# Optimization experiments

Hardware: AMD Instinct MI355X
Metric: run time of the kernel (lower is better)

The kernel has to match this reference:

```python
import jax, jax.numpy as jnp
import numpy as np

ACT_BIT = 3
W_BIT = 2


def fake_quant(x, bits):
    """Symmetric uniform fake-quantization to `bits` bits (dequantized values)."""
    qmax = float((1 << (bits - 1)) - 1)
    scale = jnp.max(jnp.abs(x)) / qmax
    scale = jnp.where(scale == 0, jnp.ones_like(scale), scale)
    return jnp.clip(jnp.round(x / scale), -qmax, qmax) * scale


def setup_inputs() -> dict:
    key = jax.random.key(0)
    kA, kX, kWi, kWo = jax.random.split(key, 4)
    N, D_IN, D_H, D_OUT = 8192, 128, 64, 16
    A = jax.random.normal(kA, (N, N), dtype=jnp.float32)       # dense subgraph adjacency (binarized inside)
    X = jax.random.normal(kX, (N, D_IN), dtype=jnp.float32)    # node features
    W_in = jax.random.normal(kWi, (D_IN, D_H), dtype=jnp.float32)
    W_out = jax.random.normal(kWo, (D_H, D_OUT), dtype=jnp.float32)
    return {"A": A, "X": X, "W_in": W_in, "W_out": W_out}


def reference(A, X, W_in, W_out):
    # QGTC GCNConv_Qnt: A quantized to 1 bit, activations to act_bit, weights to w_bit.
    Aq = (A > 0).astype(A.dtype)                 # 1-bit adjacency (bit_qnt(A, 1))
    Xq = fake_quant(X, ACT_BIT)                  # X_Qnt
    Wi = fake_quant(W_in, W_BIT)                 # weight_Qnt
    Wo = fake_quant(W_out, W_BIT)
    # Layer 1: mm_v1(X, W_in) then mm_v1(A, .) with output re-quantized to act_bit
    h = Aq @ (Xq @ Wi)                           # [N, D_H]
    hq = fake_quant(h, ACT_BIT)
    # Layer 2 (output layer)
    out = Aq @ (hq @ Wo)                         # [N, D_OUT]
    return out
```

## Files before the change

kernel.cpp:

```cpp
#include <hip/hip_runtime.h>

#define NN 8192
#define DIN 128
#define DH 64
#define DOUT 16
#define KS 8

typedef _Float16 half8 __attribute__((ext_vector_type(8)));
typedef float f32x4 __attribute__((ext_vector_type(4)));

#define OFF_SC    0u
#define OFF_PART  256u
#define OFF_YT    65536u
#define OFF_RT    1114112u
#define OFF_HF    1376256u
#define OFF_BITS  3473408u
#define OFF_P1    11862016u

__device__ __forceinline__ int permk(int k) {
  int e = k & 255;
  return (k & ~255) | (((e & 3) << 6) | (e >> 2));
}

__device__ __forceinline__ float getscale(const unsigned* sc, int idx, float qmax) {
  float s = __uint_as_float(sc[idx]) / qmax;
  return (s == 0.0f) ? 1.0f : s;
}

__device__ __forceinline__ half8 expand8(unsigned bb) {
  uint4 w;
  w.x = ((bb & 1u)  ? 0x3C00u : 0u) | ((bb & 2u)   ? 0x3C000000u : 0u);
  w.y = ((bb & 4u)  ? 0x3C00u : 0u) | ((bb & 8u)   ? 0x3C000000u : 0u);
  w.z = ((bb & 16u) ? 0x3C00u : 0u) | ((bb & 32u)  ? 0x3C000000u : 0u);
  w.w = ((bb & 64u) ? 0x3C00u : 0u) | ((bb & 128u) ? 0x3C000000u : 0u);
  return __builtin_bit_cast(half8, w);
}

__global__ __launch_bounds__(256) void k_scalesbits(const float* __restrict__ A,
                                                    const float* __restrict__ X,
                                                    const float* __restrict__ Wi,
                                                    const float* __restrict__ Wo,
                                                    unsigned char* __restrict__ bits,
                                                    unsigned* part, unsigned* sc) {
  const int t = threadIdx.x, bx = blockIdx.x;
  if (bx < 4096) {
    const int lane = t & 63, warp = t >> 6;
    const size_t wbase = ((size_t)bx * 4 + warp) * 4096;
    const float4* ap = (const float4*)(A + wbase) + lane;
    unsigned char* bp = bits + (wbase >> 3);
#pragma unroll
    for (int g = 0; g < 16; ++g) {
      float4 v = ap[g * 64];
      unsigned long long m0 = __ballot(v.x > 0.0f);
      unsigned long long m1 = __ballot(v.y > 0.0f);
      unsigned long long m2 = __ballot(v.z > 0.0f);
      unsigned long long m3 = __ballot(v.w > 0.0f);
      unsigned long long lo = (lane & 1) ? m1 : m0;
      unsigned long long hi = (lane & 1) ? m3 : m2;
      unsigned long long word = (lane & 2) ? hi : lo;
      if (lane < 4) *(unsigned long long*)(bp + g * 32 + lane * 8) = word;
    }
    return;
  }
  __shared__ float red[256];
  const int b = bx - 4096;
  float m = 0.0f;
  if (b < 240) {
    for (int i = b * 256 + t; i < NN * DIN; i += 240 * 256) m = fmaxf(m, fabsf(X[i]));
  } else if (b == 240) {
    for (int i = t; i < DIN * DH; i += 256) m = fmaxf(m, fabsf(Wi[i]));
    if (t == 0) sc[3] = 0u;
  } else {
    for (int i = t; i < DH * DOUT; i += 256) m = fmaxf(m, fabsf(Wo[i]));
  }
  red[t] = m; __syncthreads();
  for (int s = 128; s > 0; s >>= 1) {
    if (t < s) red[t] = fmaxf(red[t], red[t + s]);
    __syncthreads();
  }
  if (t == 0) part[b] = __float_as_uint(red[0]);
}

__global__ __launch_bounds__(256) void k_Y(const float* __restrict__ X,
                                           const float* __restrict__ Wi,
                                           const unsigned* __restrict__ part,
                                           unsigned* sc,
                                           _Float16* __restrict__ YT) {
  __shared__ float red[256];
  __shared__ float Xs[8][129];
  __shared__ float Ws[DIN][DH];
  const int t = threadIdx.x;
  red[t] = (t < 240) ? __uint_as_float(part[t]) : 0.0f;
  __syncthreads();
  for (int s = 128; s > 0; s >>= 1) {
    if (t < s) red[t] = fmaxf(red[t], red[t + s]);
    __syncthreads();
  }
  float sxraw = red[0];
  float sx = sxraw / 3.0f; sx = (sx == 0.0f) ? 1.0f : sx;
  float swi = __uint_as_float(part[240]); swi = (swi == 0.0f) ? 1.0f : swi;
  if (blockIdx.x == 0 && t == 0) sc[0] = __float_as_uint(sxraw);
  const int k0 = blockIdx.x * 8;
  __syncthreads();
  for (int i = t; i < 8 * DIN; i += 256) {
    int r = i >> 7, c = i & 127;
    float q = rintf(X[(size_t)(k0 + r) * DIN + c] / sx);
    Xs[r][c] = fminf(fmaxf(q, -3.0f), 3.0f);
  }
  for (int i = t; i < DIN * DH; i += 256) {
    float q = rintf(Wi[i] / swi);
    Ws[i >> 6][i & 63] = fminf(fmaxf(q, -1.0f), 1.0f);
  }
  __syncthreads();
  const int r = t & 7, jp = t >> 3, j = jp * 2;
  float a0 = 0.0f, a1 = 0.0f;
  for (int n = 0; n < DIN; ++n) {
    float xv = Xs[r][n];
    a0 = fmaf(xv, Ws[n][j], a0);
    a1 = fmaf(xv, Ws[n][j + 1], a1);
  }
  const int kp = permk(k0 + r);
  YT[(size_t)j * NN + kp]       = (_Float16)a0;
  YT[(size_t)(j + 1) * NN + kp] = (_Float16)a1;
}

__global__ __launch_bounds__(256) void k_gemm1(const unsigned char* __restrict__ bits,
                                               const _Float16* __restrict__ YT,
                                               float* __restrict__ P1) {
  __shared__ __align__(16) char Bs[64 * 128];
  const int t = threadIdx.x, lane = t & 63, warp = t >> 6;
  const int row0 = blockIdx.x * 128;
  const int split = blockIdx.y;
  const int l15 = lane & 15, lq = lane >> 4;
  const int sh8 = lq * 8;

  f32x4 acc[2][4] = {};

  const int bn = t >> 2, bp = t & 3;
  const _Float16* bsrc = YT + (size_t)bn * NN + split * 1024 + bp * 16;
  char* bdst0 = &Bs[bn * 128 + ((bp * 32) ^ ((bn & 7) << 4))];
  char* bdst1 = &Bs[bn * 128 + ((bp * 32 + 16) ^ ((bn & 7) << 4))];

  const unsigned char* brow0 = bits + (size_t)(row0 + warp * 32 + l15) * 1024 + split * 128;
  const unsigned char* brow1 = brow0 + 16 * 1024;

  uint4 breg0 = *(const uint4*)(bsrc);
  uint4 breg1 = *(const uint4*)(bsrc + 8);

  for (int it = 0; it < 16; ++it) {
    __syncthreads();
    *(uint4*)bdst0 = breg0;
    *(uint4*)bdst1 = breg1;
    if (it < 15) {
      breg0 = *(const uint4*)(bsrc + (it + 1) * 64);
      breg1 = *(const uint4*)(bsrc + (it + 1) * 64 + 8);
    }
    uint2 w0 = *(const uint2*)(brow0 + it * 8);
    uint2 w1 = *(const uint2*)(brow1 + it * 8);
    __syncthreads();
#pragma unroll
    for (int kk = 0; kk < 2; ++kk) {
      half8 af0 = expand8(((kk ? w0.y : w0.x) >> sh8) & 0xffu);
      half8 af1 = expand8(((kk ? w1.y : w1.x) >> sh8) & 0xffu);
#pragma unroll
      for (int n = 0; n < 4; ++n) {
        half8 bf = *(const half8*)(&Bs[(n * 16 + l15) * 128 +
                                       ((lq * 16 + kk * 64) ^ ((l15 & 7) << 4))]);
        acc[0][n] = __builtin_amdgcn_mfma_f32_16x16x32_f16(af0, bf, acc[0][n], 0, 0, 0);
        acc[1][n] = __builtin_amdgcn_mfma_f32_16x16x32_f16(af1, bf, acc[1][n], 0, 0, 0);
      }
    }
  }
  const int r4 = lq * 4;
#pragma unroll
  for (int mf = 0; mf < 2; ++mf) {
#pragma unroll
    for (int n = 0; n < 4; ++n) {
#pragma unroll
      for (int i = 0; i < 4; ++i) {
        int rr = row0 + warp * 32 + mf * 16 + r4 + i;
        int cc = n * 16 + l15;
        P1[((size_t)split * NN + rr) * DH + cc] = acc[mf][n][i];
      }
    }
  }
}

__global__ __launch_bounds__(256) void k_h2(const float* __restrict__ P1,
                                            const unsigned* __restrict__ part,
                                            unsigned* sc, float* __restrict__ hf) {
  float sx = getscale(sc, 0, 3.0f);
  float swi = __uint_as_float(part[240]); swi = (swi == 0.0f) ? 1.0f : swi;
  float sxw = sx * swi;
  int idx = blockIdx.x * 256 + threadIdx.x;
  const float4* p = (const float4*)P1;
  float4 s = {0, 0, 0, 0};
#pragma unroll
  for (int sp = 0; sp < KS; ++sp) {
    float4 v = p[(size_t)sp * (NN * DH / 4) + idx];
    s.x += v.x; s.y += v.y; s.z += v.z; s.w += v.w;
  }
  s.x *= sxw; s.y *= sxw; s.z *= sxw; s.w *= sxw;
  ((float4*)hf)[idx] = s;
  float m = fmaxf(fmaxf(fabsf(s.x), fabsf(s.y)), fmaxf(fabsf(s.z), fabsf(s.w)));
  __shared__ float red[256];
  red[threadIdx.x] = m; __syncthreads();
  for (int st = 128; st > 0; st >>= 1) {
    if (threadIdx.x < st) red[threadIdx.x] = fmaxf(red[threadIdx.x], red[threadIdx.x + st]);
    __syncthreads();
  }
  if (threadIdx.x == 0) atomicMax(&sc[3], __float_as_uint(red[0]));
}

__global__ __launch_bounds__(256) void k_R(const float* __restrict__ hf,
                                           const float* __restrict__ Wo,
                                           const unsigned* __restrict__ part,
                                           const unsigned* __restrict__ sc,
                                           _Float16* __restrict__ RT) {
  __shared__ float WoS[DH][DOUT];
  float sh = getscale(sc, 3, 3.0f);
  float swo = __uint_as_float(part[241]); swo = (swo == 0.0f) ? 1.0f : swo;
  int t = threadIdx.x;
  for (int i = t; i < DH * DOUT; i += 256) {
    float q = rintf(Wo[i] / swo);
    WoS[i >> 4][i & 15] = fminf(fmaxf(q, -1.0f), 1.0f);
  }
  __syncthreads();
  int i = blockIdx.x * 16 + (t & 15), j = t >> 4;
  const float4* hp = (const float4*)(hf + (size_t)i * DH);
  float acc = 0.0f;
#pragma unroll 4
  for (int nb = 0; nb < 16; ++nb) {
    float4 h4 = hp[nb];
    float q;
    q = fminf(fmaxf(rintf(h4.x / sh), -3.0f), 3.0f); acc = fmaf(q, WoS[nb * 4 + 0][j], acc);
    q = fminf(fmaxf(rintf(h4.y / sh), -3.0f), 3.0f); acc = fmaf(q, WoS[nb * 4 + 1][j], acc);
    q = fminf(fmaxf(rintf(h4.z / sh), -3.0f), 3.0f); acc = fmaf(q, WoS[nb * 4 + 2][j], acc);
    q = fminf(fmaxf(rintf(h4.w / sh), -3.0f), 3.0f); acc = fmaf(q, WoS[nb * 4 + 3][j], acc);
  }
  RT[(size_t)j * NN + permk(i)] = (_Float16)acc;
}

__global__ __launch_bounds__(256) void k_gemm2(const unsigned char* __restrict__ bits,
                                               const _Float16* __restrict__ RT,
                                               const unsigned* __restrict__ part,
                                               const unsigned* __restrict__ sc,
                                               float* __restrict__ out) {
  __shared__ float red2[3][16][16];
  const int t = threadIdx.x, lane = t & 63, warp = t >> 6;
  const int row0 = blockIdx.x * 16;
  const int l15 = lane & 15, lq = lane >> 4;
  const int sh8 = lq * 8;

  const unsigned char* brow = bits + (size_t)(row0 + l15) * 1024 + warp * 256;
  const _Float16* rrow = RT + (size_t)l15 * NN + warp * 2048 + lq * 8;

  f32x4 acc = {};
#pragma unroll 8
  for (int it = 0; it < 32; ++it) {
    uint2 w = *(const uint2*)(brow + it * 8);
#pragma unroll
    for (int kk = 0; kk < 2; ++kk) {
      half8 af = expand8(((kk ? w.y : w.x) >> sh8) & 0xffu);
      half8 bf = *(const half8*)(rrow + it * 64 + kk * 32);
      acc = __builtin_amdgcn_mfma_f32_16x16x32_f16(af, bf, acc, 0, 0, 0);
    }
  }
  if (warp > 0) {
#pragma unroll
    for (int i = 0; i < 4; ++i) red2[warp - 1][lq * 4 + i][l15] = acc[i];
  }
  __syncthreads();
  if (warp == 0) {
    float sh = getscale(sc, 3, 3.0f);
    float swo = __uint_as_float(part[241]); swo = (swo == 0.0f) ? 1.0f : swo;
    float s = sh * swo;
#pragma unroll
    for (int i = 0; i < 4; ++i) {
      int r = lq * 4 + i;
      float v = acc[i] + red2[0][r][l15] + red2[1][r][l15] + red2[2][r][l15];
      out[(size_t)(row0 + r) * DOUT + l15] = v * s;
    }
  }
}

extern "C" void kernel_launch(void* const* d_in, const int* in_sizes, int n_in,
                              void* d_out, int out_size, void* d_ws, size_t ws_size,
                              hipStream_t stream) {
  const float* A  = (const float*)d_in[0];
  const float* X  = (const float*)d_in[1];
  const float* Wi = (const float*)d_in[2];
  const float* Wo = (const float*)d_in[3];
  char* ws = (char*)d_ws;
  unsigned* sc        = (unsigned*)(ws + OFF_SC);
  unsigned* part      = (unsigned*)(ws + OFF_PART);
  _Float16* YT        = (_Float16*)(ws + OFF_YT);
  _Float16* RT        = (_Float16*)(ws + OFF_RT);
  float* hf           = (float*)(ws + OFF_HF);
  unsigned char* bits = (unsigned char*)(ws + OFF_BITS);
  float* P1           = (float*)(ws + OFF_P1);
  float* out          = (float*)d_out;

  k_scalesbits<<<4338, 256, 0, stream>>>(A, X, Wi, Wo, bits, part, sc);
  k_Y<<<1024, 256, 0, stream>>>(X, Wi, part, sc, YT);
  k_gemm1<<<dim3(NN / 128, KS), 256, 0, stream>>>(bits, YT, P1);
  k_h2<<<NN * DH / 1024, 256, 0, stream>>>(P1, part, sc, hf);
  k_R<<<NN / 16, 256, 0, stream>>>(hf, Wo, part, sc, RT);
  k_gemm2<<<NN / 16, 256, 0, stream>>>(bits, RT, part, sc, out);
}
```

Measured before the change: 125.7 us.

## Block Y into k-major tiles and enlarge gemm1 row tile to 256

Y is now written in a blocked layout of 8-k groups by 64 columns, so gemm1 can bulk-copy a contiguous 64KB slab into LDS with simple coalesced copies in two halves instead of a per-iteration register-staged pipeline. Each block now covers 256 rows with a 4x4 MFMA tile per warp, which doubles B-operand reuse and halves the grid to 32x8 blocks. In exchange it uses 64KB of LDS per block, which lowers occupancy, and it drops the overlap of global loads with MFMA work.

```diff
diff --git a/kernel.cpp b/kernel.cpp
--- a/kernel.cpp
+++ b/kernel.cpp
@@ -85,7 +85,7 @@
                                            const float* __restrict__ Wi,
                                            const unsigned* __restrict__ part,
                                            unsigned* sc,
-                                           _Float16* __restrict__ YT) {
+                                           _Float16* __restrict__ Yb) {
   __shared__ float red[256];
   __shared__ float Xs[8][129];
   __shared__ float Ws[DIN][DH];
@@ -120,67 +120,67 @@
     a1 = fmaf(xv, Ws[n][j + 1], a1);
   }
   const int kp = permk(k0 + r);
-  YT[(size_t)j * NN + kp]       = (_Float16)a0;
-  YT[(size_t)(j + 1) * NN + kp] = (_Float16)a1;
+  const size_t base = (size_t)(kp >> 3) * 512 + (size_t)j * 8 + (kp & 7);
+  Yb[base]     = (_Float16)a0;
+  Yb[base + 8] = (_Float16)a1;
 }
 
 __global__ __launch_bounds__(256) void k_gemm1(const unsigned char* __restrict__ bits,
-                                               const _Float16* __restrict__ YT,
+                                               const _Float16* __restrict__ Yb,
                                                float* __restrict__ P1) {
-  __shared__ __align__(16) char Bs[64 * 128];
+  __shared__ __align__(16) char Ls[65536];
   const int t = threadIdx.x, lane = t & 63, warp = t >> 6;
-  const int row0 = blockIdx.x * 128;
+  const int row0 = blockIdx.x * 256;
   const int split = blockIdx.y;
   const int l15 = lane & 15, lq = lane >> 4;
   const int sh8 = lq * 8;
 
-  f32x4 acc[2][4] = {};
-
-  const int bn = t >> 2, bp = t & 3;
-  const _Float16* bsrc = YT + (size_t)bn * NN + split * 1024 + bp * 16;
-  char* bdst0 = &Bs[bn * 128 + ((bp * 32) ^ ((bn & 7) << 4))];
-  char* bdst1 = &Bs[bn * 128 + ((bp * 32 + 16) ^ ((bn & 7) << 4))];
-
-  const unsigned char* brow0 = bits + (size_t)(row0 + warp * 32 + l15) * 1024 + split * 128;
-  const unsigned char* brow1 = brow0 + 16 * 1024;
-
-  uint4 breg0 = *(const uint4*)(bsrc);
-  uint4 breg1 = *(const uint4*)(bsrc + 8);
-
-  for (int it = 0; it < 16; ++it) {
-    __syncthreads();
-    *(uint4*)bdst0 = breg0;
-    *(uint4*)bdst1 = breg1;
-    if (it < 15) {
-      breg0 = *(const uint4*)(bsrc + (it + 1) * 64);
-      breg1 = *(const uint4*)(bsrc + (it + 1) * 64 + 8);
-    }
-    uint2 w0 = *(const uint2*)(brow0 + it * 8);
-    uint2 w1 = *(const uint2*)(brow1 + it * 8);
-    __syncthreads();
-#pragma unroll
-    for (int kk = 0; kk < 2; ++kk) {
-      half8 af0 = expand8(((kk ? w0.y : w0.x) >> sh8) & 0xffu);
-      half8 af1 = expand8(((kk ? w1.y : w1.x) >> sh8) & 0xffu);
-#pragma unroll
-      for (int n = 0; n < 4; ++n) {
-        half8 bf = *(const half8*)(&Bs[(n * 16 + l15) * 128 +
-                                       ((lq * 16 + kk * 64) ^ ((l15 & 7) << 4))]);
-        acc[0][n] = __builtin_amdgcn_mfma_f32_16x16x32_f16(af0, bf, acc[0][n], 0, 0, 0);
-        acc[1][n] = __builtin_amdgcn_mfma_f32_16x16x32_f16(af1, bf, acc[1][n], 0, 0, 0);
+  f32x4 acc[4][4] = {};
+  const char* ysrc = (const char*)Yb + (size_t)split * 131072;
+  const unsigned char* bbase = bits + split * 128;
+
+  for (int half = 0; half < 2; ++half) {
+    __syncthreads();
+    {
+      const uint4* src = (const uint4*)(ysrc + half * 65536) + t;
+      uint4* dst = (uint4*)Ls + t;
+#pragma unroll
+      for (int p = 0; p < 16; ++p) dst[p * 256] = src[p * 256];
+    }
+    __syncthreads();
+#pragma unroll
+    for (int it = 0; it < 8; ++it) {
+      uint2 w[4];
+#pragma unroll
+      for (int rt = 0; rt < 4; ++rt)
+        w[rt] = *(const uint2*)(bbase +
+                 (size_t)(row0 + warp * 64 + rt * 16 + l15) * 1024 + half * 64 + it * 8);
+#pragma unroll
+      for (int kk = 0; kk < 2; ++kk) {
+        half8 bf[4];
+#pragma unroll
+        for (int nt = 0; nt < 4; ++nt)
+          bf[nt] = *(const half8*)(&Ls[(it * 8 + kk * 4 + lq) * 1024 + (nt * 16 + l15) * 16]);
+#pragma unroll
+        for (int rt = 0; rt < 4; ++rt) {
+          half8 af = expand8(((kk ? w[rt].y : w[rt].x) >> sh8) & 0xffu);
+#pragma unroll
+          for (int nt = 0; nt < 4; ++nt)
+            acc[rt][nt] = __builtin_amdgcn_mfma_f32_16x16x32_f16(af, bf[nt], acc[rt][nt], 0, 0, 0);
+        }
       }
     }
   }
   const int r4 = lq * 4;
 #pragma unroll
-  for (int mf = 0; mf < 2; ++mf) {
-#pragma unroll
-    for (int n = 0; n < 4; ++n) {
+  for (int rt = 0; rt < 4; ++rt) {
+#pragma unroll
+    for (int nt = 0; nt < 4; ++nt) {
 #pragma unroll
       for (int i = 0; i < 4; ++i) {
-        int rr = row0 + warp * 32 + mf * 16 + r4 + i;
-        int cc = n * 16 + l15;
-        P1[((size_t)split * NN + rr) * DH + cc] = acc[mf][n][i];
+        int rr = row0 + warp * 64 + rt * 16 + r4 + i;
+        int cc = nt * 16 + l15;
+        P1[((size_t)split * NN + rr) * DH + cc] = acc[rt][nt][i];
       }
     }
   }
@@ -294,7 +294,7 @@
   char* ws = (char*)d_ws;
   unsigned* sc        = (unsigned*)(ws + OFF_SC);
   unsigned* part      = (unsigned*)(ws + OFF_PART);
-  _Float16* YT        = (_Float16*)(ws + OFF_YT);
+  _Float16* Yb        = (_Float16*)(ws + OFF_YT);
   _Float16* RT        = (_Float16*)(ws + OFF_RT);
   float* hf           = (float*)(ws + OFF_HF);
   unsigned char* bits = (unsigned char*)(ws + OFF_BITS);
@@ -302,8 +302,8 @@
   float* out          = (float*)d_out;
 
   k_scalesbits<<<4338, 256, 0, stream>>>(A, X, Wi, Wo, bits, part, sc);
-  k_Y<<<1024, 256, 0, stream>>>(X, Wi, part, sc, YT);
-  k_gemm1<<<dim3(NN / 128, KS), 256, 0, stream>>>(bits, YT, P1);
+  k_Y<<<1024, 256, 0, stream>>>(X, Wi, part, sc, Yb);
+  k_gemm1<<<dim3(NN / 256, KS), 256, 0, stream>>>(bits, Yb, P1);
   k_h2<<<NN * DH / 1024, 256, 0, stream>>>(P1, part, sc, hf);
   k_R<<<NN / 16, 256, 0, stream>>>(hf, Wo, part, sc, RT);
   k_gemm2<<<NN / 16, 256, 0, stream>>>(bits, RT, part, sc, out);
```

Measured after the change: 127.0 us. About the same (+1.0%).
